# Performance work log

Hardware: AMD Instinct MI355X
Metric: run time of the kernel (lower is better)

The kernel has to match this reference:

```python
import jax, jax.numpy as jnp
import numpy as np

MARGIN = 0.3
N, D = 4096, 512
NUM_CLASSES = 64

def setup_inputs() -> dict:
    key = jax.random.key(0)
    k1, k2, k3 = jax.random.split(key, 3)
    src_feat = jax.random.normal(k1, (N, D), dtype=jnp.float32)
    tgt_feat = jax.random.normal(k2, (N, D), dtype=jnp.float32)
    labels = jax.random.randint(k3, (N,), 0, NUM_CLASSES, dtype=jnp.int64)
    return {"src_feat": src_feat, "tgt_feat": tgt_feat, "labels": labels}

def reference(src_feat, tgt_feat, labels):
    # squared Euclidean distance matrix [n, n]
    e1 = jnp.sum(src_feat * src_feat, axis=1, keepdims=True)   # [n,1]
    e2 = jnp.sum(tgt_feat * tgt_feat, axis=1, keepdims=True).T  # [1,n]
    dist = e1 + e2 - 2.0 * (src_feat @ tgt_feat.T)
    dist = jnp.maximum(dist, 0.0)  # matches dist_mat[dist_mat < 0] = 0
    # same-label mask [n, n]
    mask = labels[:, None] == labels[None, :]
    # hard positive: max dist among same-label cols; hard negative: min among others
    dist_ap = jnp.max(jnp.where(mask, dist, -jnp.inf), axis=1)  # [n]
    dist_an = jnp.min(jnp.where(mask, jnp.inf, dist), axis=1)   # [n]
    # MarginRankingLoss with target y = 1: mean(relu(-(an - ap) + margin))
    loss = jnp.mean(jax.nn.relu(dist_ap - dist_an + MARGIN))
    return loss
```

## Files before the change

kernel.cpp:

```cpp
#include <hip/hip_runtime.h>
#include <hip/hip_bf16.h>
#include <stdint.h>

#define N_PTS 4096
#define DIM 512
#define MARGIN_F 0.3f
#define POS_INF_BITS 0x7f800000

typedef short bf16x8 __attribute__((ext_vector_type(8)));
typedef float f32x4 __attribute__((ext_vector_type(4)));

__device__ __forceinline__ unsigned short f2bf(float f) {
    unsigned int b = __float_as_uint(f);
    b += 0x7FFF + ((b >> 16) & 1);
    return (unsigned short)(b >> 16);
}

__device__ __forceinline__ void async16(const unsigned short* g, unsigned short* l) {
    __builtin_amdgcn_global_load_lds(
        (const __attribute__((address_space(1))) unsigned int*)g,
        (__attribute__((address_space(3))) unsigned int*)l,
        16, 0, 0);
}

__global__ __launch_bounds__(256) void prep_kernel(
    const float* __restrict__ src, const float* __restrict__ tgt,
    unsigned short* __restrict__ src_bf, unsigned short* __restrict__ tgt_bf,
    float* __restrict__ e1, float* __restrict__ e2,
    float* __restrict__ out)
{
    const int row  = blockIdx.x * 4 + (threadIdx.x >> 6);
    const int lane = threadIdx.x & 63;

    if (blockIdx.x == 0 && threadIdx.x == 0) out[0] = 0.0f;

    const float4* s4 = (const float4*)(src + (size_t)row * DIM);
    const float4* t4 = (const float4*)(tgt + (size_t)row * DIM);
    float4 a0 = s4[lane], a1 = s4[lane + 64];
    float4 b0 = t4[lane], b1 = t4[lane + 64];

    ushort4 u;
    ushort4* so = (ushort4*)(src_bf + (size_t)row * DIM);
    ushort4* to = (ushort4*)(tgt_bf + (size_t)row * DIM);
    u.x = f2bf(a0.x); u.y = f2bf(a0.y); u.z = f2bf(a0.z); u.w = f2bf(a0.w); so[lane] = u;
    u.x = f2bf(a1.x); u.y = f2bf(a1.y); u.z = f2bf(a1.z); u.w = f2bf(a1.w); so[lane + 64] = u;
    u.x = f2bf(b0.x); u.y = f2bf(b0.y); u.z = f2bf(b0.z); u.w = f2bf(b0.w); to[lane] = u;
    u.x = f2bf(b1.x); u.y = f2bf(b1.y); u.z = f2bf(b1.z); u.w = f2bf(b1.w); to[lane + 64] = u;

    float s1 = a0.x*a0.x + a0.y*a0.y + a0.z*a0.z + a0.w*a0.w
             + a1.x*a1.x + a1.y*a1.y + a1.z*a1.z + a1.w*a1.w;
    float s2 = b0.x*b0.x + b0.y*b0.y + b0.z*b0.z + b0.w*b0.w
             + b1.x*b1.x + b1.y*b1.y + b1.z*b1.z + b1.w*b1.w;
    for (int off = 32; off; off >>= 1) {
        s1 += __shfl_down(s1, off);
        s2 += __shfl_down(s2, off);
    }
    if (lane == 0) {
        e1[row] = s1;
        e2[row] = s2;
    }
}

#define BM 128
#define BN 128
#define BK 32
#define NPART 64

__global__ __launch_bounds__(256) void dist_kernel(
    const unsigned short* __restrict__ src_bf,
    const unsigned short* __restrict__ tgt_bf,
    const float* __restrict__ e1, const float* __restrict__ e2,
    const int* __restrict__ labels,
    float* __restrict__ ap_part, float* __restrict__ an_part)
{
    __shared__ unsigned short As[BM * BK];
    __shared__ unsigned short Bs[BN * BK];
    __shared__ int   li[BM];
    __shared__ int   lj[BN];
    __shared__ float e1s[BM];
    __shared__ float e2s[BN];

    const int i0 = blockIdx.y * BM;
    const int j0 = blockIdx.x * BN;
    const int t = threadIdx.x;
    const int lane = t & 63;
    const int wave = t >> 6;

    if (t < BM) { li[t] = labels[i0 + t]; e1s[t] = e1[i0 + t]; }
    else        { int u = t - BM; lj[u] = labels[j0 + u]; e2s[u] = e2[j0 + u]; }

    const int srow = t >> 2;
    const int scol = ((t & 3) ^ ((srow >> 1) & 3)) * 8;
    const unsigned short* gA0 = src_bf + (size_t)(i0 + srow) * DIM + scol;
    const unsigned short* gA1 = src_bf + (size_t)(i0 + 64 + srow) * DIM + scol;
    const unsigned short* gB0 = tgt_bf + (size_t)(j0 + srow) * DIM + scol;
    const unsigned short* gB1 = tgt_bf + (size_t)(j0 + 64 + srow) * DIM + scol;
    unsigned short* ldsA0 = &As[0] + wave * 512;
    unsigned short* ldsA1 = &As[0] + 2048 + wave * 512;
    unsigned short* ldsB0 = &Bs[0] + wave * 512;
    unsigned short* ldsB1 = &Bs[0] + 2048 + wave * 512;

    const int wm = (wave >> 1) * 64;
    const int wn = (wave & 1) * 64;
    const int fr = lane & 15;
    const int quad = lane >> 4;
    const int fkey = (fr >> 1) & 3;

    f32x4 acc[4][4];
    #pragma unroll
    for (int a = 0; a < 4; a++)
        #pragma unroll
        for (int b = 0; b < 4; b++)
            acc[a][b] = (f32x4){0.f, 0.f, 0.f, 0.f};

    for (int kk = 0; kk < DIM; kk += BK) {
        __syncthreads();
        async16(gA0 + kk, ldsA0);
        async16(gA1 + kk, ldsA1);
        async16(gB0 + kk, ldsB0);
        async16(gB1 + kk, ldsB1);
        __syncthreads();

        bf16x8 af[4], bf[4];
        const int cp = (quad ^ fkey) * 8;
        #pragma unroll
        for (int x = 0; x < 4; x++) {
            af[x] = *(const bf16x8*)&As[(wm + x * 16 + fr) * BK + cp];
            bf[x] = *(const bf16x8*)&Bs[(wn + x * 16 + fr) * BK + cp];
        }
        #pragma unroll
        for (int tm = 0; tm < 4; tm++)
            #pragma unroll
            for (int tn = 0; tn < 4; tn++)
                acc[tm][tn] = __builtin_amdgcn_mfma_f32_16x16x32_bf16(
                    af[tm], bf[tn], acc[tm][tn], 0, 0, 0);
    }

    const float INF = __int_as_float(POS_INF_BITS);
    const int pcol = blockIdx.x * 2 + (wave & 1);
    #pragma unroll
    for (int tm = 0; tm < 4; tm++) {
        #pragma unroll
        for (int r = 0; r < 4; r++) {
            const int rl = wm + tm * 16 + quad * 4 + r;
            const float e1v = e1s[rl];
            const int   liv = li[rl];
            float apv = 0.0f;
            float anv = INF;
            #pragma unroll
            for (int tn = 0; tn < 4; tn++) {
                const int cl = wn + tn * 16 + fr;
                float d = e1v + e2s[cl] - 2.0f * acc[tm][tn][r];
                d = fmaxf(d, 0.0f);
                if (liv == lj[cl]) apv = fmaxf(apv, d);
                else               anv = fminf(anv, d);
            }
            #pragma unroll
            for (int off = 1; off < 16; off <<= 1) {
                apv = fmaxf(apv, __shfl_xor(apv, off));
                anv = fminf(anv, __shfl_xor(anv, off));
            }
            if (fr == 0) {
                ap_part[(size_t)(i0 + rl) * NPART + pcol] = apv;
                an_part[(size_t)(i0 + rl) * NPART + pcol] = anv;
            }
        }
    }
}

__global__ __launch_bounds__(128) void loss_kernel(
    const float* __restrict__ ap_part, const float* __restrict__ an_part,
    float* __restrict__ out)
{
    const int row = blockIdx.x * 128 + threadIdx.x;
    const float4* a4 = (const float4*)(ap_part + (size_t)row * NPART);
    const float4* n4 = (const float4*)(an_part + (size_t)row * NPART);
    float apv = 0.0f;
    float anv = __int_as_float(POS_INF_BITS);
    #pragma unroll
    for (int i = 0; i < NPART / 4; i++) {
        float4 a = a4[i], n = n4[i];
        apv = fmaxf(apv, fmaxf(fmaxf(a.x, a.y), fmaxf(a.z, a.w)));
        anv = fminf(anv, fminf(fminf(n.x, n.y), fminf(n.z, n.w)));
    }
    float s = fmaxf(apv - anv + MARGIN_F, 0.0f);
    for (int off = 32; off; off >>= 1) s += __shfl_down(s, off);
    __shared__ float red[2];
    if ((threadIdx.x & 63) == 0) red[threadIdx.x >> 6] = s;
    __syncthreads();
    if (threadIdx.x == 0)
        atomicAdd(out, (red[0] + red[1]) / (float)N_PTS);
}

extern "C" void kernel_launch(void* const* d_in, const int* in_sizes, int n_in,
                              void* d_out, int out_size, void* d_ws, size_t ws_size,
                              hipStream_t stream) {
    const float* src   = (const float*)d_in[0];
    const float* tgt   = (const float*)d_in[1];
    const int* labels  = (const int*)d_in[2];

    char* ws = (char*)d_ws;
    const size_t featB = (size_t)N_PTS * DIM * sizeof(unsigned short);
    unsigned short* src_bf = (unsigned short*)ws;
    unsigned short* tgt_bf = (unsigned short*)(ws + featB);
    float* e1 = (float*)(ws + 2 * featB);
    float* e2 = e1 + N_PTS;
    float* ap_part = e2 + N_PTS;
    float* an_part = ap_part + (size_t)N_PTS * NPART;

    prep_kernel<<<N_PTS / 4, 256, 0, stream>>>(src, tgt, src_bf, tgt_bf,
                                               e1, e2, (float*)d_out);
    dim3 grid(N_PTS / BN, N_PTS / BM);
    dist_kernel<<<grid, 256, 0, stream>>>(src_bf, tgt_bf, e1, e2, labels,
                                          ap_part, an_part);
    loss_kernel<<<N_PTS / 128, 128, 0, stream>>>(ap_part, an_part, (float*)d_out);
}
```

Before: 107.0 us.

## Keep full A row strip in LDS and double-buffer B across column tiles

Each workgroup now loads its entire 128x512 bf16 source strip into LDS once, with an XOR swizzle, and sweeps four 128-column target tiles. Target tiles are streamed through a double-buffered LDS slot, so only one barrier is needed per K step. The epilogue runs once per column tile, and the grid shrinks to 8x32 workgroups. This cuts repeated A loads and barrier stalls, but the roughly 150KB of LDS limits each CU to one workgroup of four waves, which weakens latency hiding.

New measurement: 124.3 us. +16.2%, slower.

```diff
diff --git a/kernel.cpp b/kernel.cpp
--- a/kernel.cpp
+++ b/kernel.cpp
@@ -6,6 +6,14 @@
 #define DIM 512
 #define MARGIN_F 0.3f
 #define POS_INF_BITS 0x7f800000
+
+#define BM 128
+#define BN 128
+#define BK 32
+#define STRIPS 8
+#define JTILES 4
+#define NPART (STRIPS * JTILES * 2)
+#define NSTEP (JTILES * (DIM / BK))
 
 typedef short bf16x8 __attribute__((ext_vector_type(8)));
 typedef float f32x4 __attribute__((ext_vector_type(4)));
@@ -61,11 +69,6 @@
     }
 }
 
-#define BM 128
-#define BN 128
-#define BK 32
-#define NPART 64
-
 __global__ __launch_bounds__(256) void dist_kernel(
     const unsigned short* __restrict__ src_bf,
     const unsigned short* __restrict__ tgt_bf,
@@ -73,38 +76,44 @@
     const int* __restrict__ labels,
     float* __restrict__ ap_part, float* __restrict__ an_part)
 {
-    __shared__ unsigned short As[BM * BK];
-    __shared__ unsigned short Bs[BN * BK];
+    __shared__ unsigned short As[BM * DIM];
+    __shared__ unsigned short Bs[2][BN * BK];
     __shared__ int   li[BM];
-    __shared__ int   lj[BN];
     __shared__ float e1s[BM];
-    __shared__ float e2s[BN];
-
-    const int i0 = blockIdx.y * BM;
-    const int j0 = blockIdx.x * BN;
-    const int t = threadIdx.x;
-    const int lane = t & 63;
-    const int wave = t >> 6;
+    __shared__ int   lj_all[JTILES * BN];
+    __shared__ float e2s_all[JTILES * BN];
+
+    const int i0    = blockIdx.y * BM;
+    const int jbase = blockIdx.x * (JTILES * BN);
+    const int t     = threadIdx.x;
+    const int lane  = t & 63;
+    const int wave  = t >> 6;
 
     if (t < BM) { li[t] = labels[i0 + t]; e1s[t] = e1[i0 + t]; }
-    else        { int u = t - BM; lj[u] = labels[j0 + u]; e2s[u] = e2[j0 + u]; }
-
-    const int srow = t >> 2;
-    const int scol = ((t & 3) ^ ((srow >> 1) & 3)) * 8;
-    const unsigned short* gA0 = src_bf + (size_t)(i0 + srow) * DIM + scol;
-    const unsigned short* gA1 = src_bf + (size_t)(i0 + 64 + srow) * DIM + scol;
-    const unsigned short* gB0 = tgt_bf + (size_t)(j0 + srow) * DIM + scol;
-    const unsigned short* gB1 = tgt_bf + (size_t)(j0 + 64 + srow) * DIM + scol;
-    unsigned short* ldsA0 = &As[0] + wave * 512;
-    unsigned short* ldsA1 = &As[0] + 2048 + wave * 512;
-    unsigned short* ldsB0 = &Bs[0] + wave * 512;
-    unsigned short* ldsB1 = &Bs[0] + 2048 + wave * 512;
+    lj_all[t]        = labels[jbase + t];
+    lj_all[t + 256]  = labels[jbase + t + 256];
+    e2s_all[t]       = e2[jbase + t];
+    e2s_all[t + 256] = e2[jbase + t + 256];
+
+    #pragma unroll
+    for (int it = 0; it < 32; it++) {
+        const int row = wave * 32 + it;
+        const unsigned short* g = src_bf + (size_t)(i0 + row) * DIM
+                                + ((lane ^ (row & 7)) * 8);
+        async16(g, &As[row * DIM]);
+    }
+
+    const int srow  = t >> 2;
+    const int scoff = ((t & 3) ^ ((srow >> 1) & 3)) * 8;
+    const unsigned short* gB0 = tgt_bf + (size_t)srow * DIM + scoff;
+    const unsigned short* gB1 = tgt_bf + (size_t)(64 + srow) * DIM + scoff;
 
     const int wm = (wave >> 1) * 64;
     const int wn = (wave & 1) * 64;
     const int fr = lane & 15;
     const int quad = lane >> 4;
-    const int fkey = (fr >> 1) & 3;
+    const int fkeyA = fr & 7;
+    const int cpB = ((quad ^ ((fr >> 1) & 3))) * 8;
 
     f32x4 acc[4][4];
     #pragma unroll
@@ -113,20 +122,35 @@
         for (int b = 0; b < 4; b++)
             acc[a][b] = (f32x4){0.f, 0.f, 0.f, 0.f};
 
-    for (int kk = 0; kk < DIM; kk += BK) {
-        __syncthreads();
-        async16(gA0 + kk, ldsA0);
-        async16(gA1 + kk, ldsA1);
-        async16(gB0 + kk, ldsB0);
-        async16(gB1 + kk, ldsB1);
-        __syncthreads();
+    {
+        const size_t off0 = (size_t)jbase * DIM;
+        async16(gB0 + off0, &Bs[0][0] + wave * 512);
+        async16(gB1 + off0, &Bs[0][0] + 2048 + wave * 512);
+    }
+    __syncthreads();
+
+    const float INF = __int_as_float(POS_INF_BITS);
+
+    #pragma unroll 4
+    for (int s = 0; s < NSTEP; s++) {
+        if (s + 1 < NSTEP) {
+            const int s1 = s + 1;
+            const size_t off = (size_t)(jbase + (s1 >> 4) * BN) * DIM
+                             + (size_t)(s1 & 15) * BK;
+            unsigned short* dst = &Bs[s1 & 1][0];
+            async16(gB0 + off, dst + wave * 512);
+            async16(gB1 + off, dst + 2048 + wave * 512);
+        }
+
+        const int k0 = s & 15;
+        const unsigned short* bb = &Bs[s & 1][0];
+        const int cpA = (((k0 << 2) | quad) ^ fkeyA) * 8;
 
         bf16x8 af[4], bf[4];
-        const int cp = (quad ^ fkey) * 8;
         #pragma unroll
         for (int x = 0; x < 4; x++) {
-            af[x] = *(const bf16x8*)&As[(wm + x * 16 + fr) * BK + cp];
-            bf[x] = *(const bf16x8*)&Bs[(wn + x * 16 + fr) * BK + cp];
+            af[x] = *(const bf16x8*)&As[(wm + x * 16 + fr) * DIM + cpA];
+            bf[x] = *(const bf16x8*)&bb[(wn + x * 16 + fr) * BK + cpB];
         }
         #pragma unroll
         for (int tm = 0; tm < 4; tm++)
@@ -134,37 +158,45 @@
             for (int tn = 0; tn < 4; tn++)
                 acc[tm][tn] = __builtin_amdgcn_mfma_f32_16x16x32_bf16(
                     af[tm], bf[tn], acc[tm][tn], 0, 0, 0);
-    }
-
-    const float INF = __int_as_float(POS_INF_BITS);
-    const int pcol = blockIdx.x * 2 + (wave & 1);
-    #pragma unroll
-    for (int tm = 0; tm < 4; tm++) {
-        #pragma unroll
-        for (int r = 0; r < 4; r++) {
-            const int rl = wm + tm * 16 + quad * 4 + r;
-            const float e1v = e1s[rl];
-            const int   liv = li[rl];
-            float apv = 0.0f;
-            float anv = INF;
+
+        if (k0 == 15) {
+            const int jt = s >> 4;
+            const int pcol = (blockIdx.x * JTILES + jt) * 2 + (wave & 1);
             #pragma unroll
-            for (int tn = 0; tn < 4; tn++) {
-                const int cl = wn + tn * 16 + fr;
-                float d = e1v + e2s[cl] - 2.0f * acc[tm][tn][r];
-                d = fmaxf(d, 0.0f);
-                if (liv == lj[cl]) apv = fmaxf(apv, d);
-                else               anv = fminf(anv, d);
+            for (int tm = 0; tm < 4; tm++) {
+                #pragma unroll
+                for (int r = 0; r < 4; r++) {
+                    const int rl = wm + tm * 16 + quad * 4 + r;
+                    const float e1v = e1s[rl];
+                    const int   liv = li[rl];
+                    float apv = 0.0f, anv = INF;
+                    #pragma unroll
+                    for (int tn = 0; tn < 4; tn++) {
+                        const int cl = jt * BN + wn + tn * 16 + fr;
+                        float d = e1v + e2s_all[cl] - 2.0f * acc[tm][tn][r];
+                        d = fmaxf(d, 0.0f);
+                        if (liv == lj_all[cl]) apv = fmaxf(apv, d);
+                        else                   anv = fminf(anv, d);
+                    }
+                    #pragma unroll
+                    for (int off = 1; off < 16; off <<= 1) {
+                        apv = fmaxf(apv, __shfl_xor(apv, off));
+                        anv = fminf(anv, __shfl_xor(anv, off));
+                    }
+                    if (fr == 0) {
+                        ap_part[(size_t)(i0 + rl) * NPART + pcol] = apv;
+                        an_part[(size_t)(i0 + rl) * NPART + pcol] = anv;
+                    }
+                }
             }
             #pragma unroll
-            for (int off = 1; off < 16; off <<= 1) {
-                apv = fmaxf(apv, __shfl_xor(apv, off));
-                anv = fminf(anv, __shfl_xor(anv, off));
-            }
-            if (fr == 0) {
-                ap_part[(size_t)(i0 + rl) * NPART + pcol] = apv;
-                an_part[(size_t)(i0 + rl) * NPART + pcol] = anv;
-            }
+            for (int a = 0; a < 4; a++)
+                #pragma unroll
+                for (int b = 0; b < 4; b++)
+                    acc[a][b] = (f32x4){0.f, 0.f, 0.f, 0.f};
         }
+
+        __syncthreads();
     }
 }
 
@@ -210,7 +242,7 @@
 
     prep_kernel<<<N_PTS / 4, 256, 0, stream>>>(src, tgt, src_bf, tgt_bf,
                                                e1, e2, (float*)d_out);
-    dim3 grid(N_PTS / BN, N_PTS / BM);
+    dim3 grid(STRIPS, N_PTS / BM);
     dist_kernel<<<grid, 256, 0, stream>>>(src_bf, tgt_bf, e1, e2, labels,
                                           ap_part, an_part);
     loss_kernel<<<N_PTS / 128, 128, 0, stream>>>(ap_part, an_part, (float*)d_out);
```

## Double-buffer LDS tiles with async prefetch in distance GEMM loop

Applied to the files above, without the earlier changes.

The K loop now uses two LDS buffers per operand and issues the global-to-LDS loads for the next K step before computing the current one. It waits with explicit vmcnt counts and raw s_barrier instead of two __syncthreads per step, so memory latency can overlap the MFMA work. LDS use doubles to 32KB for the tiles, which may lower occupancy. The hand-written waitcnt and barrier asm also risks ordering problems, because the LDS reads before each barrier are not explicitly waited on with lgkmcnt.

Measured after the change: 102.0 us. 4.7% less time.

```diff
diff --git a/kernel.cpp b/kernel.cpp
--- a/kernel.cpp
+++ b/kernel.cpp
@@ -22,6 +22,10 @@
         (__attribute__((address_space(3))) unsigned int*)l,
         16, 0, 0);
 }
+
+#define RAW_BARRIER()  asm volatile("s_barrier" ::: "memory")
+#define WAIT_VM4()     asm volatile("s_waitcnt vmcnt(4)" ::: "memory")
+#define WAIT_VM0()     asm volatile("s_waitcnt vmcnt(0)" ::: "memory")
 
 __global__ __launch_bounds__(256) void prep_kernel(
     const float* __restrict__ src, const float* __restrict__ tgt,
@@ -64,6 +68,7 @@
 #define BM 128
 #define BN 128
 #define BK 32
+#define NSTEP (DIM / BK)
 #define NPART 64
 
 __global__ __launch_bounds__(256) void dist_kernel(
@@ -73,8 +78,8 @@
     const int* __restrict__ labels,
     float* __restrict__ ap_part, float* __restrict__ an_part)
 {
-    __shared__ unsigned short As[BM * BK];
-    __shared__ unsigned short Bs[BN * BK];
+    __shared__ unsigned short As[2][BM * BK];
+    __shared__ unsigned short Bs[2][BN * BK];
     __shared__ int   li[BM];
     __shared__ int   lj[BN];
     __shared__ float e1s[BM];
@@ -95,16 +100,15 @@
     const unsigned short* gA1 = src_bf + (size_t)(i0 + 64 + srow) * DIM + scol;
     const unsigned short* gB0 = tgt_bf + (size_t)(j0 + srow) * DIM + scol;
     const unsigned short* gB1 = tgt_bf + (size_t)(j0 + 64 + srow) * DIM + scol;
-    unsigned short* ldsA0 = &As[0] + wave * 512;
-    unsigned short* ldsA1 = &As[0] + 2048 + wave * 512;
-    unsigned short* ldsB0 = &Bs[0] + wave * 512;
-    unsigned short* ldsB1 = &Bs[0] + 2048 + wave * 512;
+    const int ldsOff0 = wave * 512;
+    const int ldsOff1 = 2048 + wave * 512;
 
     const int wm = (wave >> 1) * 64;
     const int wn = (wave & 1) * 64;
     const int fr = lane & 15;
     const int quad = lane >> 4;
     const int fkey = (fr >> 1) & 3;
+    const int cp = (quad ^ fkey) * 8;
 
     f32x4 acc[4][4];
     #pragma unroll
@@ -113,20 +117,33 @@
         for (int b = 0; b < 4; b++)
             acc[a][b] = (f32x4){0.f, 0.f, 0.f, 0.f};
 
-    for (int kk = 0; kk < DIM; kk += BK) {
-        __syncthreads();
-        async16(gA0 + kk, ldsA0);
-        async16(gA1 + kk, ldsA1);
-        async16(gB0 + kk, ldsB0);
-        async16(gB1 + kk, ldsB1);
-        __syncthreads();
-
+    async16(gA0, &As[0][0] + ldsOff0);
+    async16(gA1, &As[0][0] + ldsOff1);
+    async16(gB0, &Bs[0][0] + ldsOff0);
+    async16(gB1, &Bs[0][0] + ldsOff1);
+
+    #pragma unroll
+    for (int s = 0; s < NSTEP; s++) {
+        if (s + 1 < NSTEP) {
+            const int kk = (s + 1) * BK;
+            const int nb = (s + 1) & 1;
+            async16(gA0 + kk, &As[nb][0] + ldsOff0);
+            async16(gA1 + kk, &As[nb][0] + ldsOff1);
+            async16(gB0 + kk, &Bs[nb][0] + ldsOff0);
+            async16(gB1 + kk, &Bs[nb][0] + ldsOff1);
+            WAIT_VM4();
+        } else {
+            WAIT_VM0();
+        }
+        RAW_BARRIER();
+
+        const unsigned short* aa = &As[s & 1][0];
+        const unsigned short* bb = &Bs[s & 1][0];
         bf16x8 af[4], bf[4];
-        const int cp = (quad ^ fkey) * 8;
         #pragma unroll
         for (int x = 0; x < 4; x++) {
-            af[x] = *(const bf16x8*)&As[(wm + x * 16 + fr) * BK + cp];
-            bf[x] = *(const bf16x8*)&Bs[(wn + x * 16 + fr) * BK + cp];
+            af[x] = *(const bf16x8*)&aa[(wm + x * 16 + fr) * BK + cp];
+            bf[x] = *(const bf16x8*)&bb[(wn + x * 16 + fr) * BK + cp];
         }
         #pragma unroll
         for (int tm = 0; tm < 4; tm++)
@@ -134,6 +151,9 @@
             for (int tn = 0; tn < 4; tn++)
                 acc[tm][tn] = __builtin_amdgcn_mfma_f32_16x16x32_bf16(
                     af[tm], bf[tn], acc[tm][tn], 0, 0, 0);
+
+        if (s + 1 < NSTEP)
+            RAW_BARRIER();
     }
 
     const float INF = __int_as_float(POS_INF_BITS);
```

## Replace LDS-tiled GEMM with single-wave blocks loading MFMA fragments from global

Applied to the files above, without the earlier changes.

The dist kernel now launches one-wave blocks that each own a 128x64 output tile and load bf16 MFMA operand fragments straight from global memory into registers, skipping LDS staging and __syncthreads. The next K-step's fragments are prefetched into registers while the current step's MFMAs run. Labels and norms are read directly from global. The aim is to remove barrier and LDS overhead, at the cost of more global/L2 traffic (no operand sharing across waves), strided uncoalesced 16-byte loads, and high register pressure from the 8x4 accumulator tile plus double-buffered fragments.

After: 128.3 us. 1.2x slower.

```diff
diff --git a/kernel.cpp b/kernel.cpp
--- a/kernel.cpp
+++ b/kernel.cpp
@@ -14,13 +14,6 @@
     unsigned int b = __float_as_uint(f);
     b += 0x7FFF + ((b >> 16) & 1);
     return (unsigned short)(b >> 16);
-}
-
-__device__ __forceinline__ void async16(const unsigned short* g, unsigned short* l) {
-    __builtin_amdgcn_global_load_lds(
-        (const __attribute__((address_space(1))) unsigned int*)g,
-        (__attribute__((address_space(3))) unsigned int*)l,
-        16, 0, 0);
 }
 
 __global__ __launch_bounds__(256) void prep_kernel(
@@ -62,98 +55,100 @@
 }
 
 #define BM 128
-#define BN 128
+#define WN 64
 #define BK 32
+#define NSTEP (DIM / BK)
 #define NPART 64
 
-__global__ __launch_bounds__(256) void dist_kernel(
+__global__ __launch_bounds__(64, 2) void dist_kernel(
     const unsigned short* __restrict__ src_bf,
     const unsigned short* __restrict__ tgt_bf,
     const float* __restrict__ e1, const float* __restrict__ e2,
     const int* __restrict__ labels,
     float* __restrict__ ap_part, float* __restrict__ an_part)
 {
-    __shared__ unsigned short As[BM * BK];
-    __shared__ unsigned short Bs[BN * BK];
-    __shared__ int   li[BM];
-    __shared__ int   lj[BN];
-    __shared__ float e1s[BM];
-    __shared__ float e2s[BN];
-
     const int i0 = blockIdx.y * BM;
-    const int j0 = blockIdx.x * BN;
-    const int t = threadIdx.x;
-    const int lane = t & 63;
-    const int wave = t >> 6;
-
-    if (t < BM) { li[t] = labels[i0 + t]; e1s[t] = e1[i0 + t]; }
-    else        { int u = t - BM; lj[u] = labels[j0 + u]; e2s[u] = e2[j0 + u]; }
-
-    const int srow = t >> 2;
-    const int scol = ((t & 3) ^ ((srow >> 1) & 3)) * 8;
-    const unsigned short* gA0 = src_bf + (size_t)(i0 + srow) * DIM + scol;
-    const unsigned short* gA1 = src_bf + (size_t)(i0 + 64 + srow) * DIM + scol;
-    const unsigned short* gB0 = tgt_bf + (size_t)(j0 + srow) * DIM + scol;
-    const unsigned short* gB1 = tgt_bf + (size_t)(j0 + 64 + srow) * DIM + scol;
-    unsigned short* ldsA0 = &As[0] + wave * 512;
-    unsigned short* ldsA1 = &As[0] + 2048 + wave * 512;
-    unsigned short* ldsB0 = &Bs[0] + wave * 512;
-    unsigned short* ldsB1 = &Bs[0] + 2048 + wave * 512;
-
-    const int wm = (wave >> 1) * 64;
-    const int wn = (wave & 1) * 64;
+    const int j0 = blockIdx.x * WN;
+    const int lane = threadIdx.x;
     const int fr = lane & 15;
     const int quad = lane >> 4;
-    const int fkey = (fr >> 1) & 3;
-
-    f32x4 acc[4][4];
-    #pragma unroll
-    for (int a = 0; a < 4; a++)
+
+    const unsigned short* aBase = src_bf + (size_t)(i0 + fr) * DIM + quad * 8;
+    const unsigned short* bBase = tgt_bf + (size_t)(j0 + fr) * DIM + quad * 8;
+
+    f32x4 acc[8][4];
+    #pragma unroll
+    for (int a = 0; a < 8; a++)
         #pragma unroll
         for (int b = 0; b < 4; b++)
             acc[a][b] = (f32x4){0.f, 0.f, 0.f, 0.f};
 
-    for (int kk = 0; kk < DIM; kk += BK) {
-        __syncthreads();
-        async16(gA0 + kk, ldsA0);
-        async16(gA1 + kk, ldsA1);
-        async16(gB0 + kk, ldsB0);
-        async16(gB1 + kk, ldsB1);
-        __syncthreads();
-
-        bf16x8 af[4], bf[4];
-        const int cp = (quad ^ fkey) * 8;
+    bf16x8 afc[8], bfc[4];
+    #pragma unroll
+    for (int x = 0; x < 8; x++)
+        afc[x] = *(const bf16x8*)(aBase + (size_t)x * 16 * DIM);
+    #pragma unroll
+    for (int x = 0; x < 4; x++)
+        bfc[x] = *(const bf16x8*)(bBase + (size_t)x * 16 * DIM);
+
+    #pragma unroll
+    for (int s = 0; s < NSTEP; s++) {
+        bf16x8 afn[8], bfn[4];
+        if (s + 1 < NSTEP) {
+            const int ko = (s + 1) * BK;
+            #pragma unroll
+            for (int x = 0; x < 8; x++)
+                afn[x] = *(const bf16x8*)(aBase + (size_t)x * 16 * DIM + ko);
+            #pragma unroll
+            for (int x = 0; x < 4; x++)
+                bfn[x] = *(const bf16x8*)(bBase + (size_t)x * 16 * DIM + ko);
+        }
+
         #pragma unroll
-        for (int x = 0; x < 4; x++) {
-            af[x] = *(const bf16x8*)&As[(wm + x * 16 + fr) * BK + cp];
-            bf[x] = *(const bf16x8*)&Bs[(wn + x * 16 + fr) * BK + cp];
-        }
-        #pragma unroll
-        for (int tm = 0; tm < 4; tm++)
+        for (int tm = 0; tm < 8; tm++)
             #pragma unroll
             for (int tn = 0; tn < 4; tn++)
                 acc[tm][tn] = __builtin_amdgcn_mfma_f32_16x16x32_bf16(
-                    af[tm], bf[tn], acc[tm][tn], 0, 0, 0);
+                    afc[tm], bfc[tn], acc[tm][tn], 0, 0, 0);
+
+        if (s + 1 < NSTEP) {
+            #pragma unroll
+            for (int x = 0; x < 8; x++) afc[x] = afn[x];
+            #pragma unroll
+            for (int x = 0; x < 4; x++) bfc[x] = bfn[x];
+        }
+    }
+
+    float4 e14[8]; int4 li4[8];
+    #pragma unroll
+    for (int tm = 0; tm < 8; tm++) {
+        e14[tm] = *(const float4*)(e1 + i0 + tm * 16 + quad * 4);
+        li4[tm] = *(const int4*)(labels + i0 + tm * 16 + quad * 4);
+    }
+    float e2v[4]; int ljv[4];
+    #pragma unroll
+    for (int tn = 0; tn < 4; tn++) {
+        e2v[tn] = e2[j0 + tn * 16 + fr];
+        ljv[tn] = labels[j0 + tn * 16 + fr];
     }
 
     const float INF = __int_as_float(POS_INF_BITS);
-    const int pcol = blockIdx.x * 2 + (wave & 1);
-    #pragma unroll
-    for (int tm = 0; tm < 4; tm++) {
+    const int pcol = blockIdx.x;
+    #pragma unroll
+    for (int tm = 0; tm < 8; tm++) {
         #pragma unroll
         for (int r = 0; r < 4; r++) {
-            const int rl = wm + tm * 16 + quad * 4 + r;
-            const float e1v = e1s[rl];
-            const int   liv = li[rl];
+            const int rl = tm * 16 + quad * 4 + r;
+            const float e1v = ((const float*)&e14[tm])[r];
+            const int   liv = ((const int*)&li4[tm])[r];
             float apv = 0.0f;
             float anv = INF;
             #pragma unroll
             for (int tn = 0; tn < 4; tn++) {
-                const int cl = wn + tn * 16 + fr;
-                float d = e1v + e2s[cl] - 2.0f * acc[tm][tn][r];
+                float d = e1v + e2v[tn] - 2.0f * acc[tm][tn][r];
                 d = fmaxf(d, 0.0f);
-                if (liv == lj[cl]) apv = fmaxf(apv, d);
-                else               anv = fminf(anv, d);
+                if (liv == ljv[tn]) apv = fmaxf(apv, d);
+                else                anv = fminf(anv, d);
             }
             #pragma unroll
             for (int off = 1; off < 16; off <<= 1) {
@@ -210,8 +205,8 @@
 
     prep_kernel<<<N_PTS / 4, 256, 0, stream>>>(src, tgt, src_bf, tgt_bf,
                                                e1, e2, (float*)d_out);
-    dim3 grid(N_PTS / BN, N_PTS / BM);
-    dist_kernel<<<grid, 256, 0, stream>>>(src_bf, tgt_bf, e1, e2, labels,
-                                          ap_part, an_part);
+    dim3 grid(N_PTS / WN, N_PTS / BM);
+    dist_kernel<<<grid, 64, 0, stream>>>(src_bf, tgt_bf, e1, e2, labels,
+                                         ap_part, an_part);
     loss_kernel<<<N_PTS / 128, 128, 0, stream>>>(ap_part, an_part, (float*)d_out);
 }
```
